# Performance work log

Hardware: AMD Instinct MI355X
Metric: run time of the kernel (lower is better)

## Reference

```python
import jax, jax.numpy as jnp
import numpy as np

NNODES = 8192
K = 512
NEG_SLOPE = 0.01  # torch F.leaky_relu default
EPS = 1e-12       # torch F.normalize default eps


def setup_inputs() -> dict:
    key = jax.random.key(0)
    kx, kp = jax.random.split(key)
    x = jax.random.normal(kx, (NNODES, K), dtype=jnp.float32)
    # xavier_uniform init for proto (nnodes, k)
    bound = float(np.sqrt(6.0 / (NNODES + K)))
    proto = jax.random.uniform(kp, (NNODES, K), dtype=jnp.float32,
                               minval=-bound, maxval=bound)
    return {"x": x, "proto": proto}


def reference(x, proto):
    # In-place no_grad step in torch: proto <- l2norm(proto), rows unit-norm.
    norm = jnp.sqrt(jnp.sum(proto * proto, axis=1, keepdims=True))
    pn = proto / jnp.maximum(norm, EPS)  # (nnodes, k), unit rows
    # cosine_similarity over all pairs == pn @ pn.T since rows are unit-norm.
    # This fuses torch's (nnodes, nnodes, k) broadcast into one GEMM.
    sim = jnp.einsum('ik,jk->ij', pn, pn)  # (nnodes, nnodes)
    return jnp.where(sim >= 0, sim, NEG_SLOPE * sim)
```

## Files before the change

kernel.cpp:

```cpp
#include <hip/hip_runtime.h>
#include <stdint.h>

#define NN 8192
#define KD 512
#define BM 128
#define BK 32
#define NTILE (NN / BM)
#define NTRI (NTILE * (NTILE + 1) / 2)
#define NKT (KD / BK)

typedef __bf16 bf16;
typedef __bf16 bf16x8 __attribute__((ext_vector_type(8)));
typedef float f32x4 __attribute__((ext_vector_type(4)));

__global__ __launch_bounds__(256) void rownorm_kernel(const float* __restrict__ proto,
                                                      bf16* __restrict__ pn) {
    const int row  = blockIdx.x * 4 + (threadIdx.x >> 6);
    const int lane = threadIdx.x & 63;
    const float4* src = (const float4*)(proto + (size_t)row * KD) + lane * 2;
    const float4 v0 = src[0];
    const float4 v1 = src[1];
    float s = v0.x*v0.x + v0.y*v0.y + v0.z*v0.z + v0.w*v0.w
            + v1.x*v1.x + v1.y*v1.y + v1.z*v1.z + v1.w*v1.w;
#pragma unroll
    for (int off = 32; off; off >>= 1) s += __shfl_xor(s, off);
    const float inv = 1.0f / fmaxf(sqrtf(s), 1e-12f);
    bf16x8 o;
    o[0] = (bf16)(v0.x*inv); o[1] = (bf16)(v0.y*inv);
    o[2] = (bf16)(v0.z*inv); o[3] = (bf16)(v0.w*inv);
    o[4] = (bf16)(v1.x*inv); o[5] = (bf16)(v1.y*inv);
    o[6] = (bf16)(v1.z*inv); o[7] = (bf16)(v1.w*inv);
    *(bf16x8*)(pn + (size_t)row * KD + lane * 8) = o;
}

__device__ __forceinline__ void gload_lds16(const bf16* g, bf16* l) {
    __builtin_amdgcn_global_load_lds(
        (const __attribute__((address_space(1))) void*)g,
        (__attribute__((address_space(3))) void*)l, 16, 0, 0);
}

__device__ __forceinline__ float lrelu(float v) {
    return (v >= 0.0f) ? v : 0.01f * v;
}

__global__ __launch_bounds__(256, 4) void gemm_sym_kernel(const bf16* __restrict__ P,
                                                          float* __restrict__ C) {
    __shared__ __align__(16) unsigned char smem[33024];
    bf16*  sA = (bf16*)smem;
    bf16*  sB = (bf16*)(smem + 16384);
    float* sE = (float*)smem;

    const int bid = blockIdx.x;
    const int swz = (bid & 7) * (NTRI / 8) + (bid >> 3);
    int tm = 0, rem = swz;
    while (rem >= NTILE - tm) { rem -= NTILE - tm; ++tm; }
    const int tn = tm + rem;

    const int tid  = threadIdx.x;
    const int w    = tid >> 6;
    const int lane = tid & 63;
    const int wr = w >> 1;
    const int rowA0 = tm * BM;
    const int rowB0 = tn * BM;
    const int wm = wr * 64;
    const int wn = (w & 1) * 64;
    const int rr = lane & 15;
    const int h  = lane >> 4;

    const int chunk0 = w * 128 + lane;
    const bf16* g0 = P + (size_t)(chunk0 >> 2) * KD + (chunk0 & 3) * 8;
    const size_t offA = (size_t)rowA0 * KD;
    const size_t offB = (size_t)rowB0 * KD;
    const int ldsOff0 = w * 1024;
    const int ldsOff1 = w * 1024 + 512;

    f32x4 acc[4][4] = {};

#define STAGE(buf, kt)                                                        \
    do {                                                                      \
        gload_lds16(g0 + offA + (kt),           sA + (buf) * 4096 + ldsOff0); \
        gload_lds16(g0 + offA + 16 * KD + (kt), sA + (buf) * 4096 + ldsOff1); \
        gload_lds16(g0 + offB + (kt),           sB + (buf) * 4096 + ldsOff0); \
        gload_lds16(g0 + offB + 16 * KD + (kt), sB + (buf) * 4096 + ldsOff1); \
    } while (0)

#define COMPUTE(buf)                                                          \
    do {                                                                      \
        const bf16* ra_ = sA + (buf) * 4096;                                  \
        const bf16* rb_ = sB + (buf) * 4096;                                  \
        bf16x8 af[4], bfr[4];                                                 \
        _Pragma("unroll")                                                     \
        for (int m = 0; m < 4; ++m)                                           \
            af[m] = *(const bf16x8*)(ra_ + (wm + m * 16 + rr) * 32 + h * 8);  \
        _Pragma("unroll")                                                     \
        for (int n = 0; n < 4; ++n)                                           \
            bfr[n] = *(const bf16x8*)(rb_ + (wn + n * 16 + rr) * 32 + h * 8); \
        _Pragma("unroll")                                                     \
        for (int m = 0; m < 4; ++m)                                           \
            _Pragma("unroll")                                                 \
            for (int n = 0; n < 4; ++n)                                       \
                acc[m][n] = __builtin_amdgcn_mfma_f32_16x16x32_bf16(          \
                    af[m], bfr[n], acc[m][n], 0, 0, 0);                       \
    } while (0)

    STAGE(0, 0);
    __syncthreads();

#pragma unroll
    for (int t = 0; t < NKT; ++t) {
        if (t < NKT - 1) STAGE((t + 1) & 1, (t + 1) * BK);
        COMPUTE(t & 1);
        if (t < NKT - 1) __syncthreads();
    }

    const int cr = h * 4;
    const int cc = rr;

#pragma unroll
    for (int H = 0; H < 2; ++H) {
        __syncthreads();
        if (wr == H) {
#pragma unroll
            for (int m = 0; m < 4; ++m)
#pragma unroll
                for (int n = 0; n < 4; ++n)
#pragma unroll
                    for (int r = 0; r < 4; ++r)
                        sE[(m * 16 + cr + r) * 129 + wn + n * 16 + cc] =
                            lrelu(acc[m][n][r]);
        }
        __syncthreads();

#pragma unroll
        for (int k = 0; k < 8; ++k) {
            const int seg = tid + k * 256;
            const int lr  = seg >> 5;
            const int c4  = (seg & 31) * 4;
            const float4 v = *(const float4*)&sE[lr * 129 + c4];
            *(float4*)&C[(size_t)(rowA0 + H * 64 + lr) * NN + rowB0 + c4] = v;
        }

        if (tm != tn) {
#pragma unroll
            for (int rd = 0; rd < 8; ++rd) {
                const int j = (tid >> 4) + rd * 16;
                const int i0 = (tid & 15) * 4;
                float4 v;
                v.x = sE[(i0 + 0) * 129 + j];
                v.y = sE[(i0 + 1) * 129 + j];
                v.z = sE[(i0 + 2) * 129 + j];
                v.w = sE[(i0 + 3) * 129 + j];
                *(float4*)&C[(size_t)(rowB0 + j) * NN + rowA0 + H * 64 + i0] = v;
            }
        }
    }
#undef STAGE
#undef COMPUTE
}

extern "C" void kernel_launch(void* const* d_in, const int* in_sizes, int n_in,
                              void* d_out, int out_size, void* d_ws, size_t ws_size,
                              hipStream_t stream) {
    const float* proto = (const float*)d_in[1];
    float* C  = (float*)d_out;
    bf16* pn  = (bf16*)d_ws;

    rownorm_kernel<<<dim3(NN / 4), dim3(256), 0, stream>>>(proto, pn);
    gemm_sym_kernel<<<dim3(NTRI), dim3(256), 0, stream>>>(pn, C);
}
```

Before: 94.05 us.

## Stage transposed tile separately, use LDS-only barriers and nontemporal output stores

The epilogue swaps `__syncthreads` for barriers that wait only on LDS counters. Barriers then no longer stall on outstanding global stores. The mirrored (transposed) half of each symmetric tile is now written to LDS in a second, column-major pass, so it can be read back with vector loads instead of four scalar gathers. All output writes become nontemporal stores to reduce cache pollution. The cost is one extra LDS write pass and extra barriers, and the stride-65 layout may produce misaligned 16-byte LDS accesses.

```diff
diff --git a/kernel.cpp b/kernel.cpp
--- a/kernel.cpp
+++ b/kernel.cpp
@@ -45,10 +45,11 @@
 
 __global__ __launch_bounds__(256, 4) void gemm_sym_kernel(const bf16* __restrict__ P,
                                                           float* __restrict__ C) {
-    __shared__ __align__(16) unsigned char smem[33024];
+    __shared__ __align__(16) unsigned char smem[33280];
     bf16*  sA = (bf16*)smem;
     bf16*  sB = (bf16*)(smem + 16384);
     float* sE = (float*)smem;
+    float* sM = (float*)smem;
 
     const int bid = blockIdx.x;
     const int swz = (bid & 7) * (NTRI / 8) + (bid >> 3);
@@ -116,9 +117,15 @@
     const int cr = h * 4;
     const int cc = rr;
 
+#define LGKM0_BAR()                                                   \
+    do {                                                              \
+        asm volatile("s_waitcnt lgkmcnt(0)" ::: "memory");            \
+        __builtin_amdgcn_s_barrier();                                 \
+    } while (0)
+
 #pragma unroll
     for (int H = 0; H < 2; ++H) {
-        __syncthreads();
+        LGKM0_BAR();
         if (wr == H) {
 #pragma unroll
             for (int m = 0; m < 4; ++m)
@@ -129,33 +136,48 @@
                         sE[(m * 16 + cr + r) * 129 + wn + n * 16 + cc] =
                             lrelu(acc[m][n][r]);
         }
-        __syncthreads();
+        LGKM0_BAR();
 
 #pragma unroll
         for (int k = 0; k < 8; ++k) {
             const int seg = tid + k * 256;
             const int lr  = seg >> 5;
             const int c4  = (seg & 31) * 4;
-            const float4 v = *(const float4*)&sE[lr * 129 + c4];
-            *(float4*)&C[(size_t)(rowA0 + H * 64 + lr) * NN + rowB0 + c4] = v;
+            const f32x4 v = *(const f32x4*)&sE[lr * 129 + c4];
+            __builtin_nontemporal_store(
+                v, (f32x4*)&C[(size_t)(rowA0 + H * 64 + lr) * NN + rowB0 + c4]);
         }
+        LGKM0_BAR();
+
+        if (wr == H) {
+#pragma unroll
+            for (int m = 0; m < 4; ++m)
+#pragma unroll
+                for (int n = 0; n < 4; ++n) {
+                    f32x4 tv;
+                    tv[0] = lrelu(acc[m][n][0]);
+                    tv[1] = lrelu(acc[m][n][1]);
+                    tv[2] = lrelu(acc[m][n][2]);
+                    tv[3] = lrelu(acc[m][n][3]);
+                    *(f32x4*)&sM[(wn + n * 16 + cc) * 65 + m * 16 + cr] = tv;
+                }
+        }
+        LGKM0_BAR();
 
         if (tm != tn) {
 #pragma unroll
             for (int rd = 0; rd < 8; ++rd) {
-                const int j = (tid >> 4) + rd * 16;
+                const int j  = (tid >> 4) + rd * 16;
                 const int i0 = (tid & 15) * 4;
-                float4 v;
-                v.x = sE[(i0 + 0) * 129 + j];
-                v.y = sE[(i0 + 1) * 129 + j];
-                v.z = sE[(i0 + 2) * 129 + j];
-                v.w = sE[(i0 + 3) * 129 + j];
-                *(float4*)&C[(size_t)(rowB0 + j) * NN + rowA0 + H * 64 + i0] = v;
+                const f32x4 v = *(const f32x4*)&sM[j * 65 + i0];
+                __builtin_nontemporal_store(
+                    v, (f32x4*)&C[(size_t)(rowB0 + j) * NN + rowA0 + H * 64 + i0]);
             }
         }
     }
 #undef STAGE
 #undef COMPUTE
+#undef LGKM0_BAR
 }
 
 extern "C" void kernel_launch(void* const* d_in, const int* in_sizes, int n_in,
```

Result: slower. 96.39 us (+2.5%).
